# Optimization experiments

Hardware: AMD Instinct MI355X
Metric: run time of the kernel (lower is better)

The kernel has to match this reference:

```python
import jax, jax.numpy as jnp
import numpy as np

IN_CH = 1024
HID_CH = 1024
NUM_HEADS = 16
HEAD_DIM = HID_CH // NUM_HEADS
SCALE = (HID_CH / NUM_HEADS) ** (-0.25)


def _xavier(key, shape):
    fan_out, fan_in = shape
    limit = np.sqrt(6.0 / (fan_in + fan_out)).astype(np.float32)
    return jax.random.uniform(key, shape, jnp.float32, -limit, limit)


def setup_inputs() -> dict:
    key = jax.random.key(0)
    ks = jax.random.split(key, 5)
    B, T, L = 4, 2048, 512
    inpt = jax.random.normal(ks[0], (B, IN_CH, T), jnp.float32)
    aux = jax.random.normal(ks[1], (L, IN_CH), jnp.float32)
    q_w = _xavier(ks[2], (HID_CH, IN_CH))
    q_b = jnp.zeros((HID_CH,), jnp.float32)
    kv_w = _xavier(ks[3], (2 * HID_CH, IN_CH))
    kv_b = jnp.zeros((2 * HID_CH,), jnp.float32)
    out_w = _xavier(ks[4], (IN_CH, HID_CH))
    out_b = jnp.zeros((IN_CH,), jnp.float32)
    return {"inpt": inpt, "aux": aux, "q_w": q_w, "q_b": q_b,
            "kv_w": kv_w, "kv_b": kv_b, "out_w": out_w, "out_b": out_b}


def reference(inpt, aux, q_w, q_b, kv_w, kv_b, out_w, out_b):
    # inpt: (B, C, T), aux: (L, C)
    B, C, T = inpt.shape
    x = jnp.swapaxes(inpt, -2, -1)                     # (B, T, C)
    q = (x @ q_w.T + q_b) * SCALE                      # (B, T, H*D)
    kv = aux @ kv_w.T + kv_b                           # (L, 2*H*D)
    k, v = jnp.split(kv, 2, axis=-1)
    k = k * SCALE
    q = q.reshape(B, T, NUM_HEADS, HEAD_DIM)           # (B, T, h, d)
    L = aux.shape[0]
    k = k.reshape(L, NUM_HEADS, HEAD_DIM)              # (L, h, d)
    v = v.reshape(L, NUM_HEADS, HEAD_DIM)
    e = jnp.einsum('bihd,jhd->bijh', q, k)             # (B, T, L, h)
    attn = jax.nn.softmax(e, axis=2)                   # softmax over key axis j
    out = jnp.einsum('bijh,jhd->bihd', attn, v)        # (B, T, h, d)
    out = out.reshape(B, T, HID_CH) @ out_w.T + out_b  # (B, T, C)
    return inpt + jnp.swapaxes(out, -2, -1)            # (B, C, T)
```

## Files before the change

### kernel.cpp

```cpp
#include <hip/hip_runtime.h>
#include <cstdint>
#include <cstddef>

typedef __bf16 bf16;
typedef __bf16 bf16x4 __attribute__((ext_vector_type(4)));
typedef __bf16 bf16x8 __attribute__((ext_vector_type(8)));
typedef float f32x4 __attribute__((ext_vector_type(4)));

static constexpr float SCALE_F = 0.35355339059327373f;

#define AS1 __attribute__((address_space(1)))
#define AS3 __attribute__((address_space(3)))

__device__ __forceinline__ void load_lds16(const void* g, void* l) {
  __builtin_amdgcn_global_load_lds((AS1 void*)g, (AS3 void*)l, 16, 0, 0);
}

__global__ void prep(const float* __restrict__ q_w, bf16* __restrict__ qwb,
                     const float* __restrict__ kv_w, bf16* __restrict__ kvwb,
                     const float* __restrict__ out_w, bf16* __restrict__ owb,
                     const float* __restrict__ aux, bf16* __restrict__ auxb,
                     const float* __restrict__ inpt, bf16* __restrict__ X) {
  const int bid = blockIdx.x;
  const int tid = threadIdx.x;
  if (bid < 4608) {
    int i = bid * 256 + tid;
    const float* src;
    bf16* dst;
    int off;
    if (i < 262144) { src = q_w; dst = qwb; off = i; }
    else if (i < 786432) { src = kv_w; dst = kvwb; off = i - 262144; }
    else if (i < 1048576) { src = out_w; dst = owb; off = i - 786432; }
    else { src = aux; dst = auxb; off = i - 1048576; }
    float4 v = reinterpret_cast<const float4*>(src)[off];
    bf16x4 o;
    o[0] = (bf16)v.x; o[1] = (bf16)v.y; o[2] = (bf16)v.z; o[3] = (bf16)v.w;
    reinterpret_cast<bf16x4*>(dst)[off] = o;
  } else {
    __shared__ float tile[32][33];
    int tb = bid - 4608;
    int b = tb >> 11;
    int rem = tb & 2047;
    int c0 = (rem >> 6) * 32;
    int t0 = (rem & 63) * 32;
    int tx = tid & 31, ty = tid >> 5;
    const float* src = inpt + ((size_t)b * 1024 + c0) * 2048 + t0;
#pragma unroll
    for (int i = 0; i < 4; ++i) tile[ty + i * 8][tx] = src[(size_t)(ty + i * 8) * 2048 + tx];
    __syncthreads();
    bf16* dst = X + ((size_t)b * 2048 + t0) * 1024 + c0;
#pragma unroll
    for (int i = 0; i < 4; ++i) dst[(size_t)(ty + i * 8) * 1024 + tx] = (bf16)tile[tx][ty + i * 8];
  }
}


__global__ __launch_bounds__(256, 3) void gemm_qkv(
    const bf16* __restrict__ X, const bf16* __restrict__ qwb, const float* __restrict__ q_b,
    bf16* __restrict__ Qout, const bf16* __restrict__ auxb, const bf16* __restrict__ kvwb,
    const float* __restrict__ kv_b, bf16* __restrict__ Kout, bf16* __restrict__ Vout) {
  __shared__ __align__(16) char sA[16384];
  __shared__ __align__(16) char sB[16384];
  const int tid = threadIdx.x;
  const int lane = tid & 63;
  const int wave = tid >> 6;
  const int wm = wave >> 1, wn = wave & 1;
  const int bid = blockIdx.x;
  const bool isQ = bid < 512;
  const bf16 *A, *Bw;
  const float* bias;
  int m0, n0;
  if (isQ) {
    A = X; Bw = qwb; bias = q_b;
    m0 = (bid >> 3) * 128; n0 = (bid & 7) * 128;
  } else {
    int b2 = bid - 512;
    A = auxb; Bw = kvwb; bias = kv_b;
    m0 = (b2 & 3) * 128; n0 = (b2 >> 2) * 128;
  }
  f32x4 acc[4][4] = {};

  for (int kt = 0; kt < 1024; kt += 64) {
#pragma unroll
    for (int j = 0; j < 4; ++j) {
      int i = tid + j * 256;
      int r = i >> 3, q = i & 7;
      int so = (q ^ (r & 7)) << 4;
      load_lds16((const char*)(A + (size_t)(m0 + r) * 1024 + kt) + so, sA + (size_t)i * 16);
      load_lds16((const char*)(Bw + (size_t)(n0 + r) * 1024 + kt) + so, sB + (size_t)i * 16);
    }
    asm volatile("s_waitcnt vmcnt(0)" ::: "memory");
    __syncthreads();
    bf16x8 af[4][2], bfr[4][2];
#pragma unroll
    for (int mi = 0; mi < 4; ++mi)
#pragma unroll
      for (int kk = 0; kk < 2; ++kk) {
        int rr = wm * 64 + mi * 16 + (lane & 15);
        int w = kk * 64 + ((lane >> 4) << 4);
        af[mi][kk] = *(const bf16x8*)(sA + (size_t)rr * 128 + (w ^ ((rr & 7) << 4)));
        int r2 = wn * 64 + mi * 16 + (lane & 15);
        bfr[mi][kk] = *(const bf16x8*)(sB + (size_t)r2 * 128 + (w ^ ((r2 & 7) << 4)));
      }
#pragma unroll
    for (int kk = 0; kk < 2; ++kk)
#pragma unroll
      for (int mi = 0; mi < 4; ++mi)
#pragma unroll
        for (int ni = 0; ni < 4; ++ni)
          acc[mi][ni] =
              __builtin_amdgcn_mfma_f32_16x16x32_bf16(af[mi][kk], bfr[ni][kk], acc[mi][ni], 0, 0, 0);
    __syncthreads();
  }

  float bs[4];
#pragma unroll
  for (int ni = 0; ni < 4; ++ni) bs[ni] = bias[n0 + wn * 64 + ni * 16 + (lane & 15)];

#pragma unroll
  for (int mi = 0; mi < 4; ++mi)
#pragma unroll
    for (int ni = 0; ni < 4; ++ni)
#pragma unroll
      for (int j = 0; j < 4; ++j) {
        int row = wm * 64 + mi * 16 + ((lane >> 4) << 2) + j;
        int col = wn * 64 + ni * 16 + (lane & 15);
        int m = m0 + row, n = n0 + col;
        float val = acc[mi][ni][j] + bs[ni];
        if (isQ) {
          val *= SCALE_F;
          int bb = m >> 11, t = m & 2047, hh = n >> 6, d = n & 63;
          Qout[(((size_t)(bb * 16 + hh) * 2048 + t) << 6) + d] = (bf16)val;
        } else {
          if (n < 1024) {
            int hh = n >> 6, d = n & 63;
            Kout[(((size_t)hh * 512 + m) << 6) + d] = (bf16)(val * SCALE_F);
          } else {
            int n2 = n - 1024;
            int hh = n2 >> 6, d = n2 & 63;
            int sl = (m & 0x1E0) | (((m >> 2) & 3) << 3) | (((m >> 4) & 1) << 2) | (m & 3);
            Vout[(((size_t)hh * 64 + d) << 9) + sl] = (bf16)val;
          }
        }
      }
}

__global__ __launch_bounds__(256, 2) void gemm_outres(const bf16* __restrict__ A,
                                                      const bf16* __restrict__ Bw,
                                                      const float* __restrict__ bias,
                                                      const float* __restrict__ inpt,
                                                      float* __restrict__ out) {
  __shared__ __align__(16) char smem[65536];
  char* sA = smem;
  char* sB = smem + 16384;
  const int tid = threadIdx.x;
  const int lane = tid & 63;
  const int wave = tid >> 6;
  const int wm = wave >> 1, wn = wave & 1;
  const int g = lane >> 4, lr = lane & 15;
  const int m0 = blockIdx.x * 128, n0 = blockIdx.y * 128;
  f32x4 acc[4][4] = {};

  for (int kt = 0; kt < 1024; kt += 64) {
#pragma unroll
    for (int j = 0; j < 4; ++j) {
      int i = tid + j * 256;
      int r = i >> 3, q = i & 7;
      int so = (q ^ (r & 7)) << 4;
      load_lds16((const char*)(A + (size_t)(m0 + r) * 1024 + kt) + so, sA + (size_t)i * 16);
      load_lds16((const char*)(Bw + (size_t)(n0 + r) * 1024 + kt) + so, sB + (size_t)i * 16);
    }
    asm volatile("s_waitcnt vmcnt(0)" ::: "memory");
    __syncthreads();
    bf16x8 af[4][2], bfr[4][2];
#pragma unroll
    for (int mi = 0; mi < 4; ++mi)
#pragma unroll
      for (int kk = 0; kk < 2; ++kk) {
        int rr = wm * 64 + mi * 16 + lr;
        int w = kk * 64 + (g << 4);
        af[mi][kk] = *(const bf16x8*)(sA + (size_t)rr * 128 + (w ^ ((rr & 7) << 4)));
        int r2 = wn * 64 + mi * 16 + lr;
        bfr[mi][kk] = *(const bf16x8*)(sB + (size_t)r2 * 128 + (w ^ ((r2 & 7) << 4)));
      }
#pragma unroll
    for (int kk = 0; kk < 2; ++kk)
#pragma unroll
      for (int mi = 0; mi < 4; ++mi)
#pragma unroll
        for (int ni = 0; ni < 4; ++ni)
          acc[mi][ni] =
              __builtin_amdgcn_mfma_f32_16x16x32_bf16(af[mi][kk], bfr[ni][kk], acc[mi][ni], 0, 0, 0);
    __syncthreads();
  }

  float bs[4];
#pragma unroll
  for (int ni = 0; ni < 4; ++ni) bs[ni] = bias[n0 + wn * 64 + ni * 16 + lr];

#pragma unroll
  for (int mi = 0; mi < 4; ++mi)
#pragma unroll
    for (int ni = 0; ni < 4; ++ni) {
      int c_l = wn * 64 + ni * 16 + lr;
      int tb = (wm * 64 + mi * 16 + g * 4) * 4;
      f32x4 v;
#pragma unroll
      for (int j = 0; j < 4; ++j) v[j] = acc[mi][ni][j] + bs[ni];
      *(f32x4*)(smem + (size_t)c_l * 512 + (tb ^ ((c_l & 31) << 4))) = v;
    }
  __syncthreads();

  const int c_r = tid >> 3;
  const int tcol = (tid & 7) * 16;
  const int b = m0 >> 11, m0t = m0 & 2047;
#pragma unroll
  for (int p = 0; p < 4; ++p) {
    int c = p * 32 + c_r;
    size_t grow = ((size_t)b * 1024 + n0 + c) * 2048 + m0t;
#pragma unroll
    for (int q = 0; q < 4; ++q) {
      int t = tcol + q * 128;
      f32x4 z = *(const f32x4*)(smem + (size_t)c * 512 + (t ^ ((c & 31) << 4)));
      f32x4 iv = *(const f32x4*)(inpt + grow + (t >> 2));
      f32x4 w;
#pragma unroll
      for (int j = 0; j < 4; ++j) w[j] = iv[j] + z[j];
      *(f32x4*)(out + grow + (t >> 2)) = w;
    }
  }
}

struct Frags {
  bf16x8 ka[2][2];
  bf16x8 va[4];
};

__device__ __forceinline__ void load_frags(Frags& f, const char* lds, int G, int lr, int g) {
  const int swz = (lr & 7) << 4;
#pragma unroll
  for (int m = 0; m < 2; ++m)
#pragma unroll
    for (int kk = 0; kk < 2; ++kk)
      f.ka[m][kk] =
          *(const bf16x8*)(lds + (size_t)(G * 32 + m * 16 + lr) * 128 + ((kk * 64 + g * 16) ^ swz));
#pragma unroll
  for (int db = 0; db < 4; ++db)
    f.va[db] = *(const bf16x8*)(lds + 65536 + (size_t)(db * 16 + lr) * 1024 +
                                ((G * 64 + g * 16) ^ swz));
}

__device__ __forceinline__ void compute_group(const Frags& f, const bf16x8 (&qf)[4][2],
                                              f32x4 (&oacc)[4][4], float (&psum)[4]) {
  f32x4 sa[4][2] = {};
#pragma unroll
  for (int s = 0; s < 4; ++s)
#pragma unroll
    for (int m = 0; m < 2; ++m) {
      sa[s][m] = __builtin_amdgcn_mfma_f32_16x16x32_bf16(f.ka[m][0], qf[s][0], sa[s][m], 0, 0, 0);
      sa[s][m] = __builtin_amdgcn_mfma_f32_16x16x32_bf16(f.ka[m][1], qf[s][1], sa[s][m], 0, 0, 0);
    }
  bf16x8 pb[4];
#pragma unroll
  for (int s = 0; s < 4; ++s)
#pragma unroll
    for (int m = 0; m < 2; ++m)
#pragma unroll
      for (int j = 0; j < 4; ++j) {
        float p = __expf(sa[s][m][j] - 16.0f);
        psum[s] += p;
        pb[s][m * 4 + j] = (bf16)p;
      }
#pragma unroll
  for (int s = 0; s < 4; ++s)
#pragma unroll
    for (int db = 0; db < 4; ++db)
      oacc[s][db] = __builtin_amdgcn_mfma_f32_16x16x32_bf16(f.va[db], pb[s], oacc[s][db], 0, 0, 0);
}

__global__ __launch_bounds__(512, 2) void attn_kernel(const bf16* __restrict__ Q,
                                                      const bf16* __restrict__ Kw,
                                                      const bf16* __restrict__ Vt,
                                                      bf16* __restrict__ Y) {
  __shared__ __align__(16) char lds[131072];
  const int tid = threadIdx.x;
  const int lane = tid & 63;
  const int wv = tid >> 6;
  const int g = lane >> 4, lr = lane & 15;
  const int bix = blockIdx.x;
  const int b = bix >> 6, h = (bix >> 2) & 15, tc = bix & 3;

  const bf16* Kh = Kw + (size_t)h * 512 * 64;
  const bf16* Vh = Vt + (size_t)h * 64 * 512;
#pragma unroll
  for (int j = 0; j < 8; ++j) {
    int i = tid + j * 512;
    int r = i >> 3, c = i & 7;
    load_lds16((const char*)Kh + r * 128 + ((c * 16) ^ ((r & 7) << 4)), lds + (size_t)i * 16);
  }
#pragma unroll
  for (int j = 0; j < 8; ++j) {
    int i = tid + j * 512;
    int r = i >> 6, c = i & 63;
    load_lds16((const char*)Vh + r * 1024 + ((c * 16) ^ ((r & 7) << 4)),
               lds + 65536 + (size_t)i * 16);
  }

  const int tb = tc * 512 + wv * 64;
  const bf16* Qh = Q + ((size_t)(b * 16 + h) * 2048 + tb) * 64;
  bf16x8 qf[4][2];
#pragma unroll
  for (int s = 0; s < 4; ++s)
#pragma unroll
    for (int kk = 0; kk < 2; ++kk)
      qf[s][kk] = *(const bf16x8*)((const char*)Qh + (s * 16 + lr) * 128 + kk * 64 + g * 16);

  asm volatile("s_waitcnt vmcnt(0)" ::: "memory");
  __syncthreads();

  f32x4 oacc[4][4] = {};
  float psum[4] = {};

  Frags fA, fB;
  load_frags(fA, lds, 0, lr, g);
#pragma unroll 1
  for (int G = 0; G < 16; G += 2) {
    load_frags(fB, lds, G + 1, lr, g);
    compute_group(fA, qf, oacc, psum);
    if (G + 2 < 16) load_frags(fA, lds, G + 2, lr, g);
    compute_group(fB, qf, oacc, psum);
  }

#pragma unroll
  for (int s = 0; s < 4; ++s) {
    float ssum = psum[s];
    ssum += __shfl_xor(ssum, 16);
    ssum += __shfl_xor(ssum, 32);
    float inv = 1.0f / ssum;
    int t = tb + s * 16 + lr;
    char* yrow = (char*)Y + ((size_t)(b * 2048 + t) * 1024 + h * 64) * 2;
#pragma unroll
    for (int db = 0; db < 4; ++db) {
      bf16x4 w;
#pragma unroll
      for (int j = 0; j < 4; ++j) w[j] = (bf16)(oacc[s][db][j] * inv);
      *(bf16x4*)(yrow + (db * 16 + g * 4) * 2) = w;
    }
  }
}


extern "C" void kernel_launch(void* const* d_in, const int* in_sizes, int n_in, void* d_out,
                              int out_size, void* d_ws, size_t ws_size, hipStream_t stream) {
  const float* inpt = (const float*)d_in[0];
  const float* aux = (const float*)d_in[1];
  const float* q_w = (const float*)d_in[2];
  const float* q_b = (const float*)d_in[3];
  const float* kv_w = (const float*)d_in[4];
  const float* kv_b = (const float*)d_in[5];
  const float* out_w = (const float*)d_in[6];
  const float* out_b = (const float*)d_in[7];
  float* out = (float*)d_out;
  char* ws = (char*)d_ws;
  bf16* X = (bf16*)(ws + 0);
  bf16* QZ = (bf16*)(ws + (16u << 20));
  bf16* qwb = (bf16*)(ws + (32u << 20));
  bf16* kvwb = (bf16*)(ws + (34u << 20));
  bf16* owb = (bf16*)(ws + (38u << 20));
  bf16* auxb = (bf16*)(ws + (40u << 20));
  bf16* Kws = (bf16*)(ws + (41u << 20));
  bf16* Vtw = (bf16*)(ws + (42u << 20));

  prep<<<12800, 256, 0, stream>>>(q_w, qwb, kv_w, kvwb, out_w, owb, aux, auxb, inpt, X);
  gemm_qkv<<<576, 256, 0, stream>>>(X, qwb, q_b, QZ, auxb, kvwb, kv_b, Kws, Vtw);
  attn_kernel<<<256, 512, 0, stream>>>(QZ, Kws, Vtw, X );
  gemm_outres<<<dim3(64, 8), 256, 0, stream>>>(X, owb, out_b, inpt, out);
}
```

Measured before the change: 194.1 us.

## Split KV projection into its own kernel that converts fp32 inputs on load

The aux and kv_w fp32-to-bf16 conversion moves out of the prep kernel and into a new gemm_kv kernel, which reads fp32 directly and converts while staging into LDS. The combined qkv GEMM is split into separate gemm_kv (64 blocks) and gemm_q (512 blocks) launches. This drops a round trip through the workspace for the kv weights and aux, but gemm_kv now runs as a separate launch with only 64 blocks and no async LDS loads, so the GPU is underfilled while it runs.

```diff
diff --git a/kernel.cpp b/kernel.cpp
--- a/kernel.cpp
+++ b/kernel.cpp
@@ -17,28 +17,24 @@
 }
 
 __global__ void prep(const float* __restrict__ q_w, bf16* __restrict__ qwb,
-                     const float* __restrict__ kv_w, bf16* __restrict__ kvwb,
                      const float* __restrict__ out_w, bf16* __restrict__ owb,
-                     const float* __restrict__ aux, bf16* __restrict__ auxb,
                      const float* __restrict__ inpt, bf16* __restrict__ X) {
   const int bid = blockIdx.x;
   const int tid = threadIdx.x;
-  if (bid < 4608) {
+  if (bid < 2048) {
     int i = bid * 256 + tid;
     const float* src;
     bf16* dst;
     int off;
     if (i < 262144) { src = q_w; dst = qwb; off = i; }
-    else if (i < 786432) { src = kv_w; dst = kvwb; off = i - 262144; }
-    else if (i < 1048576) { src = out_w; dst = owb; off = i - 786432; }
-    else { src = aux; dst = auxb; off = i - 1048576; }
+    else { src = out_w; dst = owb; off = i - 262144; }
     float4 v = reinterpret_cast<const float4*>(src)[off];
     bf16x4 o;
     o[0] = (bf16)v.x; o[1] = (bf16)v.y; o[2] = (bf16)v.z; o[3] = (bf16)v.w;
     reinterpret_cast<bf16x4*>(dst)[off] = o;
   } else {
     __shared__ float tile[32][33];
-    int tb = bid - 4608;
+    int tb = bid - 2048;
     int b = tb >> 11;
     int rem = tb & 2047;
     int c0 = (rem >> 6) * 32;
@@ -54,11 +50,93 @@
   }
 }
 
-
-__global__ __launch_bounds__(256, 3) void gemm_qkv(
-    const bf16* __restrict__ X, const bf16* __restrict__ qwb, const float* __restrict__ q_b,
-    bf16* __restrict__ Qout, const bf16* __restrict__ auxb, const bf16* __restrict__ kvwb,
-    const float* __restrict__ kv_b, bf16* __restrict__ Kout, bf16* __restrict__ Vout) {
+__global__ __launch_bounds__(256, 2) void gemm_kv(const float* __restrict__ aux,
+                                                  const float* __restrict__ kv_w,
+                                                  const float* __restrict__ kv_b,
+                                                  bf16* __restrict__ Kout,
+                                                  bf16* __restrict__ Vout) {
+  __shared__ __align__(16) char sA[16384];
+  __shared__ __align__(16) char sB[16384];
+  const int tid = threadIdx.x;
+  const int lane = tid & 63;
+  const int wave = tid >> 6;
+  const int wm = wave >> 1, wn = wave & 1;
+  const int m0 = (blockIdx.x & 3) * 128, n0 = (blockIdx.x >> 2) * 128;
+  f32x4 acc[4][4] = {};
+
+  for (int kt = 0; kt < 1024; kt += 64) {
+#pragma unroll
+    for (int j = 0; j < 8; ++j) {
+      int v = tid + j * 256;
+      int r = v >> 4, cq = v & 15;
+      f32x4 a4 = *(const f32x4*)(aux + (size_t)(m0 + r) * 1024 + kt + cq * 4);
+      bf16x4 o;
+#pragma unroll
+      for (int e = 0; e < 4; ++e) o[e] = (bf16)a4[e];
+      *(bf16x4*)(sA + (size_t)r * 128 + ((cq * 8) ^ ((r & 7) << 4))) = o;
+    }
+#pragma unroll
+    for (int j = 0; j < 8; ++j) {
+      int v = tid + j * 256;
+      int r = v >> 4, cq = v & 15;
+      f32x4 b4 = *(const f32x4*)(kv_w + (size_t)(n0 + r) * 1024 + kt + cq * 4);
+      bf16x4 o;
+#pragma unroll
+      for (int e = 0; e < 4; ++e) o[e] = (bf16)b4[e];
+      *(bf16x4*)(sB + (size_t)r * 128 + ((cq * 8) ^ ((r & 7) << 4))) = o;
+    }
+    __syncthreads();
+    bf16x8 af[4][2], bfr[4][2];
+#pragma unroll
+    for (int mi = 0; mi < 4; ++mi)
+#pragma unroll
+      for (int kk = 0; kk < 2; ++kk) {
+        int rr = wm * 64 + mi * 16 + (lane & 15);
+        int w = kk * 64 + ((lane >> 4) << 4);
+        af[mi][kk] = *(const bf16x8*)(sA + (size_t)rr * 128 + (w ^ ((rr & 7) << 4)));
+        int r2 = wn * 64 + mi * 16 + (lane & 15);
+        bfr[mi][kk] = *(const bf16x8*)(sB + (size_t)r2 * 128 + (w ^ ((r2 & 7) << 4)));
+      }
+#pragma unroll
+    for (int kk = 0; kk < 2; ++kk)
+#pragma unroll
+      for (int mi = 0; mi < 4; ++mi)
+#pragma unroll
+        for (int ni = 0; ni < 4; ++ni)
+          acc[mi][ni] =
+              __builtin_amdgcn_mfma_f32_16x16x32_bf16(af[mi][kk], bfr[ni][kk], acc[mi][ni], 0, 0, 0);
+    __syncthreads();
+  }
+
+  float bs[4];
+#pragma unroll
+  for (int ni = 0; ni < 4; ++ni) bs[ni] = kv_b[n0 + wn * 64 + ni * 16 + (lane & 15)];
+#pragma unroll
+  for (int mi = 0; mi < 4; ++mi)
+#pragma unroll
+    for (int ni = 0; ni < 4; ++ni)
+#pragma unroll
+      for (int j = 0; j < 4; ++j) {
+        int row = wm * 64 + mi * 16 + ((lane >> 4) << 2) + j;
+        int col = wn * 64 + ni * 16 + (lane & 15);
+        int m = m0 + row, n = n0 + col;
+        float val = acc[mi][ni][j] + bs[ni];
+        if (n < 1024) {
+          int hh = n >> 6, d = n & 63;
+          Kout[(((size_t)hh * 512 + m) << 6) + d] = (bf16)(val * SCALE_F);
+        } else {
+          int n2 = n - 1024;
+          int hh = n2 >> 6, d = n2 & 63;
+          int sl = (m & 0x1E0) | (((m >> 2) & 3) << 3) | (((m >> 4) & 1) << 2) | (m & 3);
+          Vout[(((size_t)hh * 64 + d) << 9) + sl] = (bf16)val;
+        }
+      }
+}
+
+__global__ __launch_bounds__(256, 3) void gemm_q(const bf16* __restrict__ X,
+                                                 const bf16* __restrict__ qwb,
+                                                 const float* __restrict__ q_b,
+                                                 bf16* __restrict__ Qout) {
   __shared__ __align__(16) char sA[16384];
   __shared__ __align__(16) char sB[16384];
   const int tid = threadIdx.x;
@@ -66,18 +144,7 @@
   const int wave = tid >> 6;
   const int wm = wave >> 1, wn = wave & 1;
   const int bid = blockIdx.x;
-  const bool isQ = bid < 512;
-  const bf16 *A, *Bw;
-  const float* bias;
-  int m0, n0;
-  if (isQ) {
-    A = X; Bw = qwb; bias = q_b;
-    m0 = (bid >> 3) * 128; n0 = (bid & 7) * 128;
-  } else {
-    int b2 = bid - 512;
-    A = auxb; Bw = kvwb; bias = kv_b;
-    m0 = (b2 & 3) * 128; n0 = (b2 >> 2) * 128;
-  }
+  const int m0 = (bid >> 3) * 128, n0 = (bid & 7) * 128;
   f32x4 acc[4][4] = {};
 
   for (int kt = 0; kt < 1024; kt += 64) {
@@ -86,8 +153,8 @@
       int i = tid + j * 256;
       int r = i >> 3, q = i & 7;
       int so = (q ^ (r & 7)) << 4;
-      load_lds16((const char*)(A + (size_t)(m0 + r) * 1024 + kt) + so, sA + (size_t)i * 16);
-      load_lds16((const char*)(Bw + (size_t)(n0 + r) * 1024 + kt) + so, sB + (size_t)i * 16);
+      load_lds16((const char*)(X + (size_t)(m0 + r) * 1024 + kt) + so, sA + (size_t)i * 16);
+      load_lds16((const char*)(qwb + (size_t)(n0 + r) * 1024 + kt) + so, sB + (size_t)i * 16);
     }
     asm volatile("s_waitcnt vmcnt(0)" ::: "memory");
     __syncthreads();
@@ -115,8 +182,7 @@
 
   float bs[4];
 #pragma unroll
-  for (int ni = 0; ni < 4; ++ni) bs[ni] = bias[n0 + wn * 64 + ni * 16 + (lane & 15)];
-
+  for (int ni = 0; ni < 4; ++ni) bs[ni] = q_b[n0 + wn * 64 + ni * 16 + (lane & 15)];
 #pragma unroll
   for (int mi = 0; mi < 4; ++mi)
 #pragma unroll
@@ -126,22 +192,9 @@
         int row = wm * 64 + mi * 16 + ((lane >> 4) << 2) + j;
         int col = wn * 64 + ni * 16 + (lane & 15);
         int m = m0 + row, n = n0 + col;
-        float val = acc[mi][ni][j] + bs[ni];
-        if (isQ) {
-          val *= SCALE_F;
-          int bb = m >> 11, t = m & 2047, hh = n >> 6, d = n & 63;
-          Qout[(((size_t)(bb * 16 + hh) * 2048 + t) << 6) + d] = (bf16)val;
-        } else {
-          if (n < 1024) {
-            int hh = n >> 6, d = n & 63;
-            Kout[(((size_t)hh * 512 + m) << 6) + d] = (bf16)(val * SCALE_F);
-          } else {
-            int n2 = n - 1024;
-            int hh = n2 >> 6, d = n2 & 63;
-            int sl = (m & 0x1E0) | (((m >> 2) & 3) << 3) | (((m >> 4) & 1) << 2) | (m & 3);
-            Vout[(((size_t)hh * 64 + d) << 9) + sl] = (bf16)val;
-          }
-        }
+        float val = (acc[mi][ni][j] + bs[ni]) * SCALE_F;
+        int bb = m >> 11, t = m & 2047, hh = n >> 6, d = n & 63;
+        Qout[(((size_t)(bb * 16 + hh) * 2048 + t) << 6) + d] = (bf16)val;
       }
 }
 
@@ -365,14 +418,13 @@
   bf16* X = (bf16*)(ws + 0);
   bf16* QZ = (bf16*)(ws + (16u << 20));
   bf16* qwb = (bf16*)(ws + (32u << 20));
-  bf16* kvwb = (bf16*)(ws + (34u << 20));
-  bf16* owb = (bf16*)(ws + (38u << 20));
-  bf16* auxb = (bf16*)(ws + (40u << 20));
-  bf16* Kws = (bf16*)(ws + (41u << 20));
-  bf16* Vtw = (bf16*)(ws + (42u << 20));
-
-  prep<<<12800, 256, 0, stream>>>(q_w, qwb, kv_w, kvwb, out_w, owb, aux, auxb, inpt, X);
-  gemm_qkv<<<576, 256, 0, stream>>>(X, qwb, q_b, QZ, auxb, kvwb, kv_b, Kws, Vtw);
+  bf16* owb = (bf16*)(ws + (34u << 20));
+  bf16* Kws = (bf16*)(ws + (36u << 20));
+  bf16* Vtw = (bf16*)(ws + (37u << 20));
+
+  prep<<<10240, 256, 0, stream>>>(q_w, qwb, out_w, owb, inpt, X);
+  gemm_kv<<<64, 256, 0, stream>>>(aux, kv_w, kv_b, Kws, Vtw);
+  gemm_q<<<512, 256, 0, stream>>>(X, qwb, q_b, QZ);
   attn_kernel<<<256, 512, 0, stream>>>(QZ, Kws, Vtw, X );
   gemm_outres<<<dim3(64, 8), 256, 0, stream>>>(X, owb, out_b, inpt, out);
 }
```

Measured after the change: 286.8 us. 1.48x slower.
